# Kernel tuning notes

Measured on AMD Instinct MI355X. Metric: run time of the kernel, lower is better.

Reference implementation:

```python
import jax, jax.numpy as jnp
import numpy as np

N_NODES = 100000
N_EDGES = 1600000
IN_FEATS = 128
H_FEATS = 128
NUM_CLASSES = 1


def setup_inputs() -> dict:
    key = jax.random.key(0)
    ks = jax.random.split(key, 12)
    node_feat = jax.random.normal(ks[0], (N_NODES, IN_FEATS), dtype=jnp.float32)
    edge_feat = jax.random.normal(ks[1], (N_EDGES, 1), dtype=jnp.float32)
    src = jax.random.randint(ks[2], (N_EDGES,), 0, N_NODES)
    dst = jax.random.randint(ks[3], (N_EDGES,), 0, N_NODES)
    d_in1 = 2 * IN_FEATS + 1
    d_mid = 2 * H_FEATS + 1
    s1 = 1.0 / np.sqrt(d_in1)
    sm = 1.0 / np.sqrt(d_mid)
    W1 = jax.random.uniform(ks[4], (d_in1, H_FEATS), jnp.float32, -s1, s1)
    b1 = jax.random.uniform(ks[5], (H_FEATS,), jnp.float32, -s1, s1)
    Wmid = jax.random.uniform(ks[6], (8, d_mid, H_FEATS), jnp.float32, -sm, sm)
    bmid = jax.random.uniform(ks[7], (8, H_FEATS), jnp.float32, -sm, sm)
    W2 = jax.random.uniform(ks[8], (d_mid, NUM_CLASSES), jnp.float32, -sm, sm)
    b2 = jax.random.uniform(ks[9], (NUM_CLASSES,), jnp.float32, -sm, sm)
    return {"node_feat": node_feat, "edge_feat": edge_feat, "src": src, "dst": dst,
            "W1": W1, "b1": b1, "Wmid": Wmid, "bmid": bmid, "W2": W2, "b2": b2}


def _sage_conv(hn, he, src, dst, W, b):
    # copy_u + sum: aggregate source node features at destination nodes
    hn_aggr = jax.ops.segment_sum(hn[src], dst, num_segments=N_NODES)
    # copy_e + sum: aggregate edge features at destination nodes -> [N, 1]
    he_aggr = jax.ops.segment_sum(he, dst, num_segments=N_NODES)
    h_total = jnp.concatenate([hn, hn_aggr, he_aggr], axis=1)
    return h_total @ W + b


def reference(node_feat, edge_feat, src, dst, W1, b1, Wmid, bmid, W2, b2):
    h = _sage_conv(node_feat, edge_feat, src, dst, W1, b1)
    h = jax.nn.relu(h) + h
    # mid layers 1-4: relu residual
    for i in range(4):
        h = _sage_conv(h, edge_feat, src, dst, Wmid[i], bmid[i])
        h = jax.nn.relu(h) + h
    # mid layer 5: sigmoid (no residual)
    h = _sage_conv(h, edge_feat, src, dst, Wmid[4], bmid[4])
    h = jax.nn.sigmoid(h)
    # mid layers 6-7: relu residual
    for i in range(5, 7):
        h = _sage_conv(h, edge_feat, src, dst, Wmid[i], bmid[i])
        h = jax.nn.relu(h) + h
    # mid layer 8: sigmoid (no residual)
    h = _sage_conv(h, edge_feat, src, dst, Wmid[7], bmid[7])
    h = jax.nn.sigmoid(h)
    # output layer
    h = _sage_conv(h, edge_feat, src, dst, W2, b2)
    return h
```

## Files before the change

### kernel.cpp

```cpp
#include <hip/hip_runtime.h>

#define N_NODES 100000
#define N_EDGES 1600000
#define HF 128
#define BCAP 64

typedef unsigned int uint;
typedef __attribute__((ext_vector_type(8))) short short8;
typedef __attribute__((ext_vector_type(4))) float f32x4;

__device__ __forceinline__ unsigned short f2bf(float f) {
    uint u = __float_as_uint(f);
    uint r = (u + 0x7fff + ((u >> 16) & 1)) >> 16;
    return (unsigned short)r;
}
__device__ __forceinline__ float bf2f(uint bits16) {
    return __uint_as_float(bits16 << 16);
}


__global__ void fill_bucket_kernel(const int* __restrict__ src, const int* __restrict__ dst,
                                   const float* __restrict__ ef, int* __restrict__ cur,
                                   int* __restrict__ cs, float* __restrict__ efb, int E) {
    int e = blockIdx.x * blockDim.x + threadIdx.x;
    if (e < E) {
        int d = dst[e];
        int p = atomicAdd(&cur[d], 1);
        if (p < BCAP) {
            cs[(size_t)d * BCAP + p] = src[e];
            efb[(size_t)d * BCAP + p] = ef[e];
        }
    }
}

__global__ void he_kernel(const float* __restrict__ efb, const int* __restrict__ cnt,
                          float* __restrict__ he) {
    int t = threadIdx.x;
    int node = blockIdx.x * 16 + (t >> 4);
    int gl = t & 15;
    if (node >= N_NODES) return;
    int cn = cnt[node]; if (cn > BCAP) cn = BCAP;
    float s = 0.f;
    for (int e = gl; e < cn; e += 16) s += efb[(size_t)node * BCAP + e];
    s += __shfl_xor(s, 1); s += __shfl_xor(s, 2);
    s += __shfl_xor(s, 4); s += __shfl_xor(s, 8);
    if (gl == 0) he[node] = s;
}


__global__ void conv_h_kernel(const float* __restrict__ in, unsigned short* __restrict__ out) {
    int i = (blockIdx.x * 256 + threadIdx.x) * 4;
    float4 v = *(const float4*)(in + i);
    uint2 o;
    o.x = (uint)f2bf(v.x) | ((uint)f2bf(v.y) << 16);
    o.y = (uint)f2bf(v.z) | ((uint)f2bf(v.w) << 16);
    *(uint2*)(out + i) = o;
}

__global__ void conv_w_kernel(const float* __restrict__ W1, const float* __restrict__ Wmid,
                              unsigned short* __restrict__ Wt) {
    int id = blockIdx.x * 256 + threadIdx.x;
    if (id >= 9 * 32768) return;
    int layer = id >> 15;
    int rem = id & 32767;
    int kc = rem >> 10;
    int c  = (rem >> 3) & 127;
    int e  = rem & 7;
    const float* Wl = (layer == 0) ? W1 : Wmid + (size_t)(layer - 1) * 257 * 128;
    Wt[(size_t)layer * 32768 + rem] = f2bf(Wl[(size_t)(kc * 8 + e) * 128 + c]);
}

__global__ void conv_wcb_kernel(const float* __restrict__ W1, const float* __restrict__ b1,
                                const float* __restrict__ Wmid, const float* __restrict__ bmid,
                                float* __restrict__ wcarr, float* __restrict__ barr) {
    int id = blockIdx.x * 256 + threadIdx.x;
    if (id >= 9 * 128) return;
    int layer = id >> 7, c = id & 127;
    const float* Wl = (layer == 0) ? W1 : Wmid + (size_t)(layer - 1) * 257 * 128;
    const float* bl = (layer == 0) ? b1 : bmid + (size_t)(layer - 1) * 128;
    wcarr[id] = Wl[256 * 128 + c];
    barr[id]  = bl[c];
}


__device__ __forceinline__ void accum8(float* a, uint4 v) {
    a[0] += bf2f(v.x & 0xffffu); a[1] += bf2f(v.x >> 16);
    a[2] += bf2f(v.y & 0xffffu); a[3] += bf2f(v.y >> 16);
    a[4] += bf2f(v.z & 0xffffu); a[5] += bf2f(v.z >> 16);
    a[6] += bf2f(v.w & 0xffffu); a[7] += bf2f(v.w >> 16);
}

__launch_bounds__(256, 3)
__global__ void fused_layer_kernel(const unsigned short* __restrict__ X,
                                   unsigned short* __restrict__ Y,
                                   const int* __restrict__ cnt,
                                   const int* __restrict__ cs,
                                   const float* __restrict__ he,
                                   const unsigned short* __restrict__ Wt,
                                   const float* __restrict__ wcarr,
                                   const float* __restrict__ barr,
                                   int mode) {
    __shared__ short gtile[128 * 128];
    int t = threadIdx.x;
    int row0 = blockIdx.x * 128;
    int gl = t & 15;
    const uint4* hu = (const uint4*)X;

    for (int pass = 0; pass < 8; ++pass) {
        int r = pass * 16 + (t >> 4);
        int node = row0 + r;
        float ax[8] = {0.f,0.f,0.f,0.f,0.f,0.f,0.f,0.f};
        float bx[8] = {0.f,0.f,0.f,0.f,0.f,0.f,0.f,0.f};
        if (node < N_NODES) {
            int cn = cnt[node]; if (cn > BCAP) cn = BCAP;
            const int* bk = cs + (size_t)node * BCAP;
            int e = 0;
            int4 s4 = make_int4(0, 0, 0, 0);
            if (e + 4 <= cn) s4 = *(const int4*)(bk + e);
            while (e + 4 <= cn) {
                int4 c4 = s4;
                int en = e + 4;
                if (en + 4 <= cn) s4 = *(const int4*)(bk + en);
                uint4 v0 = hu[(size_t)c4.x * 16 + gl];
                uint4 v1 = hu[(size_t)c4.y * 16 + gl];
                uint4 v2 = hu[(size_t)c4.z * 16 + gl];
                uint4 v3 = hu[(size_t)c4.w * 16 + gl];
                accum8(ax, v0); accum8(bx, v1); accum8(ax, v2); accum8(bx, v3);
                e = en;
            }
            for (; e < cn; ++e) {
                uint4 v = hu[(size_t)bk[e] * 16 + gl];
                accum8(ax, v);
            }
        }
        uint4 o;
        o.x = (uint)f2bf(ax[0] + bx[0]) | ((uint)f2bf(ax[1] + bx[1]) << 16);
        o.y = (uint)f2bf(ax[2] + bx[2]) | ((uint)f2bf(ax[3] + bx[3]) << 16);
        o.z = (uint)f2bf(ax[4] + bx[4]) | ((uint)f2bf(ax[5] + bx[5]) << 16);
        o.w = (uint)f2bf(ax[6] + bx[6]) | ((uint)f2bf(ax[7] + bx[7]) << 16);
        int off = r * 256 + gl * 16;
        off ^= (r & 7) << 4;
        *(uint4*)((char*)gtile + off) = o;
    }
    __syncthreads();

    int w = t >> 6, lane = t & 63;
    int l15 = lane & 15, l4 = lane >> 4;
    int rloc = (w >> 1) * 64;
    int rb = row0 + rloc;
    int cb = (w & 1) * 64;

    f32x4 acc[4][4] = {};

    #pragma unroll
    for (int ks = 0; ks < 8; ++ks) {
        int kk = (ks & 3) * 32 + l4 * 8;
        short8 a[4];
        if (ks < 4) {
            #pragma unroll
            for (int ra = 0; ra < 4; ++ra) {
                int row = rb + ra * 16 + l15;
                if (row > N_NODES - 1) row = N_NODES - 1;
                a[ra] = *(const short8*)((const short*)X + (size_t)row * 128 + kk);
            }
        } else {
            #pragma unroll
            for (int ra = 0; ra < 4; ++ra) {
                int r = rloc + ra * 16 + l15;
                int off = r * 256 + kk * 2;
                off ^= (r & 7) << 4;
                a[ra] = *(const short8*)((const char*)gtile + off);
            }
        }
        short8 b[4];
        const short* wt = (const short*)Wt + (size_t)(ks * 4 + l4) * 1024;
        #pragma unroll
        for (int cf = 0; cf < 4; ++cf) {
            int c = cb + cf * 16 + l15;
            b[cf] = *(const short8*)(wt + c * 8);
        }
        #pragma unroll
        for (int cf = 0; cf < 4; ++cf)
            #pragma unroll
            for (int ra = 0; ra < 4; ++ra)
                acc[ra][cf] = __builtin_amdgcn_mfma_f32_16x16x32_bf16(a[ra], b[cf], acc[ra][cf], 0, 0, 0);
    }

    float wcv[4], bbv[4];
    #pragma unroll
    for (int cf = 0; cf < 4; ++cf) {
        int c = cb + cf * 16 + l15;
        wcv[cf] = wcarr[c];
        bbv[cf] = barr[c];
    }
    #pragma unroll
    for (int ra = 0; ra < 4; ++ra) {
        #pragma unroll
        for (int j = 0; j < 4; ++j) {
            int row = rb + ra * 16 + l4 * 4 + j;
            if (row >= N_NODES) continue;
            float hv = he[row];
            #pragma unroll
            for (int cf = 0; cf < 4; ++cf) {
                int c = cb + cf * 16 + l15;
                float z = acc[ra][cf][j] + hv * wcv[cf] + bbv[cf];
                if (mode == 0) z += fmaxf(z, 0.f);
                else           z = 1.f / (1.f + __expf(-z));
                Y[(size_t)row * 128 + c] = f2bf(z);
            }
        }
    }
}


__global__ void dot_kernel(const unsigned short* __restrict__ h, const float* __restrict__ W2,
                           float* __restrict__ p) {
    int t = threadIdx.x;
    int node = blockIdx.x * 16 + (t >> 4);
    int gl = t & 15;
    if (node >= N_NODES) return;
    uint4 v = ((const uint4*)h)[(size_t)node * 16 + gl];
    const float* wseg = W2 + 128 + gl * 8;
    float s = bf2f(v.x & 0xffffu) * wseg[0] + bf2f(v.x >> 16) * wseg[1]
            + bf2f(v.y & 0xffffu) * wseg[2] + bf2f(v.y >> 16) * wseg[3]
            + bf2f(v.z & 0xffffu) * wseg[4] + bf2f(v.z >> 16) * wseg[5]
            + bf2f(v.w & 0xffffu) * wseg[6] + bf2f(v.w >> 16) * wseg[7];
    s += __shfl_xor(s, 1); s += __shfl_xor(s, 2);
    s += __shfl_xor(s, 4); s += __shfl_xor(s, 8);
    if (gl == 0) p[node] = s;
}

__global__ void final2_kernel(const unsigned short* __restrict__ h, const float* __restrict__ p,
                              const int* __restrict__ cnt, const int* __restrict__ cs,
                              const float* __restrict__ he, const float* __restrict__ W2,
                              const float* __restrict__ b2, float* __restrict__ out) {
    int t = threadIdx.x;
    int node = blockIdx.x * 16 + (t >> 4);
    int gl = t & 15;
    if (node >= N_NODES) return;
    uint4 v = ((const uint4*)h)[(size_t)node * 16 + gl];
    const float* wseg = W2 + gl * 8;
    float s = bf2f(v.x & 0xffffu) * wseg[0] + bf2f(v.x >> 16) * wseg[1]
            + bf2f(v.y & 0xffffu) * wseg[2] + bf2f(v.y >> 16) * wseg[3]
            + bf2f(v.z & 0xffffu) * wseg[4] + bf2f(v.z >> 16) * wseg[5]
            + bf2f(v.w & 0xffffu) * wseg[6] + bf2f(v.w >> 16) * wseg[7];
    int cn = cnt[node]; if (cn > BCAP) cn = BCAP;
    for (int e = gl; e < cn; e += 16) s += p[cs[(size_t)node * BCAP + e]];
    s += __shfl_xor(s, 1); s += __shfl_xor(s, 2);
    s += __shfl_xor(s, 4); s += __shfl_xor(s, 8);
    if (gl == 0) out[node] = s + he[node] * W2[256] + b2[0];
}


extern "C" void kernel_launch(void* const* d_in, const int* in_sizes, int n_in,
                              void* d_out, int out_size, void* d_ws, size_t ws_size,
                              hipStream_t stream) {
    const float* node_feat = (const float*)d_in[0];
    const float* edge_feat = (const float*)d_in[1];
    const int*   src  = (const int*)d_in[2];
    const int*   dst  = (const int*)d_in[3];
    const float* W1   = (const float*)d_in[4];
    const float* b1   = (const float*)d_in[5];
    const float* Wmid = (const float*)d_in[6];
    const float* bmid = (const float*)d_in[7];
    const float* W2   = (const float*)d_in[8];
    const float* b2   = (const float*)d_in[9];
    float* out = (float*)d_out;

    char* ws = (char*)d_ws;
    size_t off = 0;
    auto carve = [&](size_t bytes) {
        void* p = ws + off;
        off = (off + bytes + 255) & ~(size_t)255;
        return p;
    };
    int*   cur  = (int*)carve((size_t)N_NODES * 4);
    float* he   = (float*)carve((size_t)N_NODES * 4);
    int*   cs   = (int*)carve((size_t)N_NODES * BCAP * 4);
    float* efb  = (float*)carve((size_t)N_NODES * BCAP * 4);
    unsigned short* h0 = (unsigned short*)carve((size_t)N_NODES * HF * 2);
    unsigned short* Wt = (unsigned short*)carve((size_t)9 * 32768 * 2);
    float* wcarr = (float*)carve((size_t)9 * 128 * 4);
    float* barr  = (float*)carve((size_t)9 * 128 * 4);
    float* pbuf  = (float*)carve((size_t)N_NODES * 4);
    unsigned short* h1 = (unsigned short*)efb;
    (void)ws_size; (void)in_sizes; (void)n_in; (void)out_size;

    hipMemsetAsync(cur, 0, (size_t)N_NODES * 4, stream);
    fill_bucket_kernel<<<dim3((N_EDGES + 255) / 256), dim3(256), 0, stream>>>(
        src, dst, edge_feat, cur, cs, efb, N_EDGES);
    he_kernel<<<dim3((N_NODES + 15) / 16), dim3(256), 0, stream>>>(efb, cur, he);

    conv_h_kernel<<<dim3(12500), dim3(256), 0, stream>>>(node_feat, h0);
    conv_w_kernel<<<dim3((9 * 32768 + 255) / 256), dim3(256), 0, stream>>>(W1, Wmid, Wt);
    conv_wcb_kernel<<<dim3(5), dim3(256), 0, stream>>>(W1, b1, Wmid, bmid, wcarr, barr);

    const int gemmGrid = (N_NODES + 127) / 128;
    unsigned short* hbuf[2] = { h0, h1 };

    for (int L = 0; L < 9; ++L) {
        int mode = (L == 5 || L == 8) ? 1 : 0;
        fused_layer_kernel<<<dim3(gemmGrid), dim3(256), 0, stream>>>(
            hbuf[L & 1], hbuf[(L + 1) & 1], cur, cs, he,
            Wt + (size_t)L * 32768, wcarr + L * 128, barr + L * 128, mode);
    }
    const unsigned short* hf = hbuf[1];
    dot_kernel<<<dim3((N_NODES + 15) / 16), dim3(256), 0, stream>>>(hf, W2, pbuf);
    final2_kernel<<<dim3((N_NODES + 15) / 16), dim3(256), 0, stream>>>(
        hf, pbuf, cur, cs, he, W2, b2, out);
}
```

Before: 873.5 us.

## Interleave bucket source ids with edge features and batch bucket-fill atomics

```diff
diff --git a/kernel.cpp b/kernel.cpp
--- a/kernel.cpp
+++ b/kernel.cpp
@@ -21,27 +21,35 @@
 
 __global__ void fill_bucket_kernel(const int* __restrict__ src, const int* __restrict__ dst,
                                    const float* __restrict__ ef, int* __restrict__ cur,
-                                   int* __restrict__ cs, float* __restrict__ efb, int E) {
-    int e = blockIdx.x * blockDim.x + threadIdx.x;
-    if (e < E) {
-        int d = dst[e];
-        int p = atomicAdd(&cur[d], 1);
-        if (p < BCAP) {
-            cs[(size_t)d * BCAP + p] = src[e];
-            efb[(size_t)d * BCAP + p] = ef[e];
-        }
-    }
-}
-
-__global__ void he_kernel(const float* __restrict__ efb, const int* __restrict__ cnt,
+                                   int2* __restrict__ csef) {
+    const int T = N_EDGES / 4;
+    int i = blockIdx.x * blockDim.x + threadIdx.x;
+    if (i >= T) return;
+    int d[4], s[4]; float f[4];
+    #pragma unroll
+    for (int k = 0; k < 4; ++k) {
+        int e = i + k * T;
+        d[k] = dst[e]; s[k] = src[e]; f[k] = ef[e];
+    }
+    int p[4];
+    #pragma unroll
+    for (int k = 0; k < 4; ++k) p[k] = atomicAdd(&cur[d[k]], 1);
+    #pragma unroll
+    for (int k = 0; k < 4; ++k)
+        if (p[k] < BCAP)
+            csef[(size_t)d[k] * BCAP + p[k]] = make_int2(s[k], __float_as_int(f[k]));
+}
+
+__global__ void he_kernel(const int2* __restrict__ csef, const int* __restrict__ cnt,
                           float* __restrict__ he) {
     int t = threadIdx.x;
     int node = blockIdx.x * 16 + (t >> 4);
     int gl = t & 15;
     if (node >= N_NODES) return;
     int cn = cnt[node]; if (cn > BCAP) cn = BCAP;
+    const int2* bk = csef + (size_t)node * BCAP;
     float s = 0.f;
-    for (int e = gl; e < cn; e += 16) s += efb[(size_t)node * BCAP + e];
+    for (int e = gl; e < cn; e += 16) s += __int_as_float(bk[e].y);
     s += __shfl_xor(s, 1); s += __shfl_xor(s, 2);
     s += __shfl_xor(s, 4); s += __shfl_xor(s, 8);
     if (gl == 0) he[node] = s;
@@ -90,11 +98,11 @@
     a[6] += bf2f(v.w & 0xffffu); a[7] += bf2f(v.w >> 16);
 }
 
-__launch_bounds__(256, 3)
+__launch_bounds__(256, 4)
 __global__ void fused_layer_kernel(const unsigned short* __restrict__ X,
                                    unsigned short* __restrict__ Y,
                                    const int* __restrict__ cnt,
-                                   const int* __restrict__ cs,
+                                   const int2* __restrict__ csef,
                                    const float* __restrict__ he,
                                    const unsigned short* __restrict__ Wt,
                                    const float* __restrict__ wcarr,
@@ -113,23 +121,23 @@
         float bx[8] = {0.f,0.f,0.f,0.f,0.f,0.f,0.f,0.f};
         if (node < N_NODES) {
             int cn = cnt[node]; if (cn > BCAP) cn = BCAP;
-            const int* bk = cs + (size_t)node * BCAP;
+            const int2* bk = csef + (size_t)node * BCAP;
             int e = 0;
-            int4 s4 = make_int4(0, 0, 0, 0);
-            if (e + 4 <= cn) s4 = *(const int4*)(bk + e);
+            int4 q0 = make_int4(0,0,0,0), q1 = make_int4(0,0,0,0);
+            if (e + 4 <= cn) { q0 = *(const int4*)(bk + e); q1 = *(const int4*)(bk + e + 2); }
             while (e + 4 <= cn) {
-                int4 c4 = s4;
+                int4 c0 = q0, c1 = q1;
                 int en = e + 4;
-                if (en + 4 <= cn) s4 = *(const int4*)(bk + en);
-                uint4 v0 = hu[(size_t)c4.x * 16 + gl];
-                uint4 v1 = hu[(size_t)c4.y * 16 + gl];
-                uint4 v2 = hu[(size_t)c4.z * 16 + gl];
-                uint4 v3 = hu[(size_t)c4.w * 16 + gl];
+                if (en + 4 <= cn) { q0 = *(const int4*)(bk + en); q1 = *(const int4*)(bk + en + 2); }
+                uint4 v0 = hu[(size_t)c0.x * 16 + gl];
+                uint4 v1 = hu[(size_t)c0.z * 16 + gl];
+                uint4 v2 = hu[(size_t)c1.x * 16 + gl];
+                uint4 v3 = hu[(size_t)c1.z * 16 + gl];
                 accum8(ax, v0); accum8(bx, v1); accum8(ax, v2); accum8(bx, v3);
                 e = en;
             }
             for (; e < cn; ++e) {
-                uint4 v = hu[(size_t)bk[e] * 16 + gl];
+                uint4 v = hu[(size_t)bk[e].x * 16 + gl];
                 accum8(ax, v);
             }
         }
@@ -231,7 +239,7 @@
 }
 
 __global__ void final2_kernel(const unsigned short* __restrict__ h, const float* __restrict__ p,
-                              const int* __restrict__ cnt, const int* __restrict__ cs,
+                              const int* __restrict__ cnt, const int2* __restrict__ csef,
                               const float* __restrict__ he, const float* __restrict__ W2,
                               const float* __restrict__ b2, float* __restrict__ out) {
     int t = threadIdx.x;
@@ -245,7 +253,8 @@
             + bf2f(v.z & 0xffffu) * wseg[4] + bf2f(v.z >> 16) * wseg[5]
             + bf2f(v.w & 0xffffu) * wseg[6] + bf2f(v.w >> 16) * wseg[7];
     int cn = cnt[node]; if (cn > BCAP) cn = BCAP;
-    for (int e = gl; e < cn; e += 16) s += p[cs[(size_t)node * BCAP + e]];
+    const int2* bk = csef + (size_t)node * BCAP;
+    for (int e = gl; e < cn; e += 16) s += p[bk[e].x];
     s += __shfl_xor(s, 1); s += __shfl_xor(s, 2);
     s += __shfl_xor(s, 4); s += __shfl_xor(s, 8);
     if (gl == 0) out[node] = s + he[node] * W2[256] + b2[0];
@@ -276,20 +285,19 @@
     };
     int*   cur  = (int*)carve((size_t)N_NODES * 4);
     float* he   = (float*)carve((size_t)N_NODES * 4);
-    int*   cs   = (int*)carve((size_t)N_NODES * BCAP * 4);
-    float* efb  = (float*)carve((size_t)N_NODES * BCAP * 4);
+    int2*  csef = (int2*)carve((size_t)N_NODES * BCAP * 8);
     unsigned short* h0 = (unsigned short*)carve((size_t)N_NODES * HF * 2);
+    unsigned short* h1 = (unsigned short*)carve((size_t)N_NODES * HF * 2);
     unsigned short* Wt = (unsigned short*)carve((size_t)9 * 32768 * 2);
     float* wcarr = (float*)carve((size_t)9 * 128 * 4);
     float* barr  = (float*)carve((size_t)9 * 128 * 4);
     float* pbuf  = (float*)carve((size_t)N_NODES * 4);
-    unsigned short* h1 = (unsigned short*)efb;
     (void)ws_size; (void)in_sizes; (void)n_in; (void)out_size;
 
     hipMemsetAsync(cur, 0, (size_t)N_NODES * 4, stream);
-    fill_bucket_kernel<<<dim3((N_EDGES + 255) / 256), dim3(256), 0, stream>>>(
-        src, dst, edge_feat, cur, cs, efb, N_EDGES);
-    he_kernel<<<dim3((N_NODES + 15) / 16), dim3(256), 0, stream>>>(efb, cur, he);
+    fill_bucket_kernel<<<dim3((N_EDGES / 4 + 255) / 256), dim3(256), 0, stream>>>(
+        src, dst, edge_feat, cur, csef);
+    he_kernel<<<dim3((N_NODES + 15) / 16), dim3(256), 0, stream>>>(csef, cur, he);
 
     conv_h_kernel<<<dim3(12500), dim3(256), 0, stream>>>(node_feat, h0);
     conv_w_kernel<<<dim3((9 * 32768 + 255) / 256), dim3(256), 0, stream>>>(W1, Wmid, Wt);
@@ -301,11 +309,11 @@
     for (int L = 0; L < 9; ++L) {
         int mode = (L == 5 || L == 8) ? 1 : 0;
         fused_layer_kernel<<<dim3(gemmGrid), dim3(256), 0, stream>>>(
-            hbuf[L & 1], hbuf[(L + 1) & 1], cur, cs, he,
+            hbuf[L & 1], hbuf[(L + 1) & 1], cur, csef, he,
             Wt + (size_t)L * 32768, wcarr + L * 128, barr + L * 128, mode);
     }
     const unsigned short* hf = hbuf[1];
     dot_kernel<<<dim3((N_NODES + 15) / 16), dim3(256), 0, stream>>>(hf, W2, pbuf);
     final2_kernel<<<dim3((N_NODES + 15) / 16), dim3(256), 0, stream>>>(
-        hf, pbuf, cur, cs, he, W2, b2, out);
-}
+        hf, pbuf, cur, csef, he, W2, b2, out);
+}
```

After: 888.6 us. About the same (+1.7%).

## Fuse edge-feature sum into bucket fill and cheapen bf16 unpack in gather

Applied to the files above, without the earlier changes.

```diff
diff --git a/kernel.cpp b/kernel.cpp
--- a/kernel.cpp
+++ b/kernel.cpp
@@ -14,37 +14,23 @@
     uint r = (u + 0x7fff + ((u >> 16) & 1)) >> 16;
     return (unsigned short)r;
 }
-__device__ __forceinline__ float bf2f(uint bits16) {
-    return __uint_as_float(bits16 << 16);
-}
 
 
 __global__ void fill_bucket_kernel(const int* __restrict__ src, const int* __restrict__ dst,
                                    const float* __restrict__ ef, int* __restrict__ cur,
-                                   int* __restrict__ cs, float* __restrict__ efb, int E) {
-    int e = blockIdx.x * blockDim.x + threadIdx.x;
-    if (e < E) {
-        int d = dst[e];
-        int p = atomicAdd(&cur[d], 1);
-        if (p < BCAP) {
-            cs[(size_t)d * BCAP + p] = src[e];
-            efb[(size_t)d * BCAP + p] = ef[e];
-        }
-    }
-}
-
-__global__ void he_kernel(const float* __restrict__ efb, const int* __restrict__ cnt,
-                          float* __restrict__ he) {
-    int t = threadIdx.x;
-    int node = blockIdx.x * 16 + (t >> 4);
-    int gl = t & 15;
-    if (node >= N_NODES) return;
-    int cn = cnt[node]; if (cn > BCAP) cn = BCAP;
-    float s = 0.f;
-    for (int e = gl; e < cn; e += 16) s += efb[(size_t)node * BCAP + e];
-    s += __shfl_xor(s, 1); s += __shfl_xor(s, 2);
-    s += __shfl_xor(s, 4); s += __shfl_xor(s, 8);
-    if (gl == 0) he[node] = s;
+                                   float* __restrict__ he, int* __restrict__ cs) {
+    const int T = N_EDGES / 2;
+    int i = blockIdx.x * blockDim.x + threadIdx.x;
+    if (i >= T) return;
+    int d0 = dst[i], d1 = dst[i + T];
+    int s0 = src[i], s1 = src[i + T];
+    float f0 = ef[i], f1 = ef[i + T];
+    int p0 = atomicAdd(&cur[d0], 1);
+    int p1 = atomicAdd(&cur[d1], 1);
+    atomicAdd(&he[d0], f0);
+    atomicAdd(&he[d1], f1);
+    if (p0 < BCAP) cs[(size_t)d0 * BCAP + p0] = s0;
+    if (p1 < BCAP) cs[(size_t)d1 * BCAP + p1] = s1;
 }
 
 
@@ -83,14 +69,14 @@
 }
 
 
-__device__ __forceinline__ void accum8(float* a, uint4 v) {
-    a[0] += bf2f(v.x & 0xffffu); a[1] += bf2f(v.x >> 16);
-    a[2] += bf2f(v.y & 0xffffu); a[3] += bf2f(v.y >> 16);
-    a[4] += bf2f(v.z & 0xffffu); a[5] += bf2f(v.z >> 16);
-    a[6] += bf2f(v.w & 0xffffu); a[7] += bf2f(v.w >> 16);
-}
-
-__launch_bounds__(256, 3)
+__device__ __forceinline__ void accum8(float* lo, float* hi, uint4 v) {
+    lo[0] += __uint_as_float(v.x << 16); hi[0] += __uint_as_float(v.x & 0xffff0000u);
+    lo[1] += __uint_as_float(v.y << 16); hi[1] += __uint_as_float(v.y & 0xffff0000u);
+    lo[2] += __uint_as_float(v.z << 16); hi[2] += __uint_as_float(v.z & 0xffff0000u);
+    lo[3] += __uint_as_float(v.w << 16); hi[3] += __uint_as_float(v.w & 0xffff0000u);
+}
+
+__launch_bounds__(256, 4)
 __global__ void fused_layer_kernel(const unsigned short* __restrict__ X,
                                    unsigned short* __restrict__ Y,
                                    const int* __restrict__ cnt,
@@ -109,35 +95,36 @@
     for (int pass = 0; pass < 8; ++pass) {
         int r = pass * 16 + (t >> 4);
         int node = row0 + r;
-        float ax[8] = {0.f,0.f,0.f,0.f,0.f,0.f,0.f,0.f};
-        float bx[8] = {0.f,0.f,0.f,0.f,0.f,0.f,0.f,0.f};
+        float alo[4] = {0.f,0.f,0.f,0.f}, ahi[4] = {0.f,0.f,0.f,0.f};
+        float blo[4] = {0.f,0.f,0.f,0.f}, bhi[4] = {0.f,0.f,0.f,0.f};
         if (node < N_NODES) {
             int cn = cnt[node]; if (cn > BCAP) cn = BCAP;
             const int* bk = cs + (size_t)node * BCAP;
             int e = 0;
-            int4 s4 = make_int4(0, 0, 0, 0);
-            if (e + 4 <= cn) s4 = *(const int4*)(bk + e);
+            int4 q = make_int4(0, 0, 0, 0);
+            if (e + 4 <= cn) q = *(const int4*)(bk + e);
             while (e + 4 <= cn) {
-                int4 c4 = s4;
+                int4 c = q;
                 int en = e + 4;
-                if (en + 4 <= cn) s4 = *(const int4*)(bk + en);
-                uint4 v0 = hu[(size_t)c4.x * 16 + gl];
-                uint4 v1 = hu[(size_t)c4.y * 16 + gl];
-                uint4 v2 = hu[(size_t)c4.z * 16 + gl];
-                uint4 v3 = hu[(size_t)c4.w * 16 + gl];
-                accum8(ax, v0); accum8(bx, v1); accum8(ax, v2); accum8(bx, v3);
+                if (en + 4 <= cn) q = *(const int4*)(bk + en);
+                uint4 v0 = hu[(size_t)c.x * 16 + gl];
+                uint4 v1 = hu[(size_t)c.y * 16 + gl];
+                uint4 v2 = hu[(size_t)c.z * 16 + gl];
+                uint4 v3 = hu[(size_t)c.w * 16 + gl];
+                accum8(alo, ahi, v0); accum8(blo, bhi, v1);
+                accum8(alo, ahi, v2); accum8(blo, bhi, v3);
                 e = en;
             }
             for (; e < cn; ++e) {
                 uint4 v = hu[(size_t)bk[e] * 16 + gl];
-                accum8(ax, v);
+                accum8(alo, ahi, v);
             }
         }
         uint4 o;
-        o.x = (uint)f2bf(ax[0] + bx[0]) | ((uint)f2bf(ax[1] + bx[1]) << 16);
-        o.y = (uint)f2bf(ax[2] + bx[2]) | ((uint)f2bf(ax[3] + bx[3]) << 16);
-        o.z = (uint)f2bf(ax[4] + bx[4]) | ((uint)f2bf(ax[5] + bx[5]) << 16);
-        o.w = (uint)f2bf(ax[6] + bx[6]) | ((uint)f2bf(ax[7] + bx[7]) << 16);
+        o.x = (uint)f2bf(alo[0] + blo[0]) | ((uint)f2bf(ahi[0] + bhi[0]) << 16);
+        o.y = (uint)f2bf(alo[1] + blo[1]) | ((uint)f2bf(ahi[1] + bhi[1]) << 16);
+        o.z = (uint)f2bf(alo[2] + blo[2]) | ((uint)f2bf(ahi[2] + bhi[2]) << 16);
+        o.w = (uint)f2bf(alo[3] + blo[3]) | ((uint)f2bf(ahi[3] + bhi[3]) << 16);
         int off = r * 256 + gl * 16;
         off ^= (r & 7) << 4;
         *(uint4*)((char*)gtile + off) = o;
@@ -213,6 +200,10 @@
 }
 
 
+__device__ __forceinline__ float bf2f_u(uint bits16) {
+    return __uint_as_float(bits16 << 16);
+}
+
 __global__ void dot_kernel(const unsigned short* __restrict__ h, const float* __restrict__ W2,
                            float* __restrict__ p) {
     int t = threadIdx.x;
@@ -221,10 +212,10 @@
     if (node >= N_NODES) return;
     uint4 v = ((const uint4*)h)[(size_t)node * 16 + gl];
     const float* wseg = W2 + 128 + gl * 8;
-    float s = bf2f(v.x & 0xffffu) * wseg[0] + bf2f(v.x >> 16) * wseg[1]
-            + bf2f(v.y & 0xffffu) * wseg[2] + bf2f(v.y >> 16) * wseg[3]
-            + bf2f(v.z & 0xffffu) * wseg[4] + bf2f(v.z >> 16) * wseg[5]
-            + bf2f(v.w & 0xffffu) * wseg[6] + bf2f(v.w >> 16) * wseg[7];
+    float s = bf2f_u(v.x & 0xffffu) * wseg[0] + bf2f_u(v.x >> 16) * wseg[1]
+            + bf2f_u(v.y & 0xffffu) * wseg[2] + bf2f_u(v.y >> 16) * wseg[3]
+            + bf2f_u(v.z & 0xffffu) * wseg[4] + bf2f_u(v.z >> 16) * wseg[5]
+            + bf2f_u(v.w & 0xffffu) * wseg[6] + bf2f_u(v.w >> 16) * wseg[7];
     s += __shfl_xor(s, 1); s += __shfl_xor(s, 2);
     s += __shfl_xor(s, 4); s += __shfl_xor(s, 8);
     if (gl == 0) p[node] = s;
@@ -240,12 +231,13 @@
     if (node >= N_NODES) return;
     uint4 v = ((const uint4*)h)[(size_t)node * 16 + gl];
     const float* wseg = W2 + gl * 8;
-    float s = bf2f(v.x & 0xffffu) * wseg[0] + bf2f(v.x >> 16) * wseg[1]
-            + bf2f(v.y & 0xffffu) * wseg[2] + bf2f(v.y >> 16) * wseg[3]
-            + bf2f(v.z & 0xffffu) * wseg[4] + bf2f(v.z >> 16) * wseg[5]
-            + bf2f(v.w & 0xffffu) * wseg[6] + bf2f(v.w >> 16) * wseg[7];
+    float s = bf2f_u(v.x & 0xffffu) * wseg[0] + bf2f_u(v.x >> 16) * wseg[1]
+            + bf2f_u(v.y & 0xffffu) * wseg[2] + bf2f_u(v.y >> 16) * wseg[3]
+            + bf2f_u(v.z & 0xffffu) * wseg[4] + bf2f_u(v.z >> 16) * wseg[5]
+            + bf2f_u(v.w & 0xffffu) * wseg[6] + bf2f_u(v.w >> 16) * wseg[7];
     int cn = cnt[node]; if (cn > BCAP) cn = BCAP;
-    for (int e = gl; e < cn; e += 16) s += p[cs[(size_t)node * BCAP + e]];
+    const int* bk = cs + (size_t)node * BCAP;
+    for (int e = gl; e < cn; e += 16) s += p[bk[e]];
     s += __shfl_xor(s, 1); s += __shfl_xor(s, 2);
     s += __shfl_xor(s, 4); s += __shfl_xor(s, 8);
     if (gl == 0) out[node] = s + he[node] * W2[256] + b2[0];
@@ -277,19 +269,18 @@
     int*   cur  = (int*)carve((size_t)N_NODES * 4);
     float* he   = (float*)carve((size_t)N_NODES * 4);
     int*   cs   = (int*)carve((size_t)N_NODES * BCAP * 4);
-    float* efb  = (float*)carve((size_t)N_NODES * BCAP * 4);
     unsigned short* h0 = (unsigned short*)carve((size_t)N_NODES * HF * 2);
+    unsigned short* h1 = (unsigned short*)carve((size_t)N_NODES * HF * 2);
     unsigned short* Wt = (unsigned short*)carve((size_t)9 * 32768 * 2);
     float* wcarr = (float*)carve((size_t)9 * 128 * 4);
     float* barr  = (float*)carve((size_t)9 * 128 * 4);
     float* pbuf  = (float*)carve((size_t)N_NODES * 4);
-    unsigned short* h1 = (unsigned short*)efb;
     (void)ws_size; (void)in_sizes; (void)n_in; (void)out_size;
 
     hipMemsetAsync(cur, 0, (size_t)N_NODES * 4, stream);
-    fill_bucket_kernel<<<dim3((N_EDGES + 255) / 256), dim3(256), 0, stream>>>(
-        src, dst, edge_feat, cur, cs, efb, N_EDGES);
-    he_kernel<<<dim3((N_NODES + 15) / 16), dim3(256), 0, stream>>>(efb, cur, he);
+    hipMemsetAsync(he, 0, (size_t)N_NODES * 4, stream);
+    fill_bucket_kernel<<<dim3((N_EDGES / 2 + 255) / 256), dim3(256), 0, stream>>>(
+        src, dst, edge_feat, cur, he, cs);
 
     conv_h_kernel<<<dim3(12500), dim3(256), 0, stream>>>(node_feat, h0);
     conv_w_kernel<<<dim3((9 * 32768 + 255) / 256), dim3(256), 0, stream>>>(W1, Wmid, Wt);
```

After: 924.3 us. 1.06x slower.
